# Kernel optimization log

Measured on AMD Instinct MI355X. Metric: run time of the kernel, lower is better.

The kernel has to match this reference:

```python
import jax, jax.numpy as jnp
import numpy as np

V, E, H, K, B, T = 50000, 128, 256, 9, 128, 512
HD = H // 2  # hidden per direction


def setup_inputs() -> dict:
    key = jax.random.key(0)
    ks = jax.random.split(key, 16)
    s = 0.1
    inp = {
        "x": jax.random.randint(ks[0], (B, T), 0, V),
        "emb": jax.random.normal(ks[1], (V, E), jnp.float32) * 0.02,
        "w_ih_f": jax.random.normal(ks[2], (4 * HD, E), jnp.float32) * s,
        "w_hh_f": jax.random.normal(ks[3], (4 * HD, HD), jnp.float32) * s,
        "b_ih_f": jax.random.normal(ks[4], (4 * HD,), jnp.float32) * s,
        "b_hh_f": jax.random.normal(ks[5], (4 * HD,), jnp.float32) * s,
        "w_ih_b": jax.random.normal(ks[6], (4 * HD, E), jnp.float32) * s,
        "w_hh_b": jax.random.normal(ks[7], (4 * HD, HD), jnp.float32) * s,
        "b_ih_b": jax.random.normal(ks[8], (4 * HD,), jnp.float32) * s,
        "b_hh_b": jax.random.normal(ks[9], (4 * HD,), jnp.float32) * s,
        "W_tag": jax.random.normal(ks[10], (K, H), jnp.float32) * s,
        "b_tag": jax.random.normal(ks[11], (K,), jnp.float32) * s,
        "start_trans": jax.random.normal(ks[12], (K,), jnp.float32) * s,
        "end_trans": jax.random.normal(ks[13], (K,), jnp.float32) * s,
        "trans": jax.random.normal(ks[14], (K, K), jnp.float32) * s,
    }
    return inp


def _lstm_dir(xs, w_ih, w_hh, b_ih, b_hh, reverse):
    # xs: [T, B, E]; PyTorch gate order: i, f, g, o
    Bsz = xs.shape[1]
    hd = w_hh.shape[1]
    b = b_ih + b_hh

    def step(carry, x_t):
        h, c = carry
        gates = x_t @ w_ih.T + h @ w_hh.T + b  # [B, 4*hd]
        i, f, g, o = jnp.split(gates, 4, axis=-1)
        i = jax.nn.sigmoid(i)
        f = jax.nn.sigmoid(f)
        g = jnp.tanh(g)
        o = jax.nn.sigmoid(o)
        c = f * c + i * g
        h = o * jnp.tanh(c)
        return (h, c), h

    init = (jnp.zeros((Bsz, hd), xs.dtype), jnp.zeros((Bsz, hd), xs.dtype))
    _, hs = jax.lax.scan(step, init, xs, reverse=reverse)
    return hs  # [T, B, hd], time-ordered


def _viterbi(emissions, start_trans, end_trans, trans):
    # emissions: [T, B, K]; returns best tag path [B, T] (torchcrf decode, no mask)
    score0 = start_trans[None, :] + emissions[0]  # [B, K]

    def step(score, emis_t):
        # score[b, i] + trans[i, j] -> best over i
        cand = score[:, :, None] + trans[None, :, :]  # [B, K, K]
        bp = jnp.argmax(cand, axis=1)                 # [B, K] best prev tag
        best = jnp.max(cand, axis=1)
        return best + emis_t, bp

    final_score, bps = jax.lax.scan(step, score0, emissions[1:])  # bps: [T-1, B, K]
    final_score = final_score + end_trans[None, :]
    last_tag = jnp.argmax(final_score, axis=-1)  # [B]

    def back(tag, bp):
        prev = jnp.take_along_axis(bp, tag[:, None], axis=1)[:, 0]
        return prev, prev

    _, path = jax.lax.scan(back, last_tag, bps, reverse=True)  # [T-1, B]
    tags = jnp.concatenate([path, last_tag[None, :]], axis=0)  # [T, B]
    return tags.T.astype(jnp.int32)  # [B, T]


def reference(x, emb, w_ih_f, w_hh_f, b_ih_f, b_hh_f,
              w_ih_b, w_hh_b, b_ih_b, b_hh_b,
              W_tag, b_tag, start_trans, end_trans, trans):
    xt = x.T                        # [T, B]
    e = emb[xt]                     # [T, B, E] embedding gather
    h_f = _lstm_dir(e, w_ih_f, w_hh_f, b_ih_f, b_hh_f, reverse=False)
    h_b = _lstm_dir(e, w_ih_b, w_hh_b, b_ih_b, b_hh_b, reverse=True)
    h = jnp.concatenate([h_f, h_b], axis=-1)  # [T, B, H]
    # dropout is identity at inference
    emissions = h @ W_tag.T + b_tag           # [T, B, K]
    return _viterbi(emissions, start_trans, end_trans, trans)
```

## Files before the change

kernel.cpp:

```cpp
#include <hip/hip_runtime.h>
#include <math.h>

#define TT 512
#define BB 128
#define KK 9

__device__ __forceinline__ float fast_sigmoid(float x) {
    const float LOG2E = 1.4426950408889634f;
    float e = __builtin_amdgcn_exp2f(-x * LOG2E);
    return __builtin_amdgcn_rcpf(1.0f + e);
}
__device__ __forceinline__ float fast_tanh(float x) {
    const float LOG2E = 1.4426950408889634f;
    float a = fabsf(x);
    float e = __builtin_amdgcn_exp2f(-2.0f * a * LOG2E);
    float t = (1.0f - e) * __builtin_amdgcn_rcpf(1.0f + e);
    return copysignf(t, x);
}

__global__ __launch_bounds__(256, 3) void input_gemm(
    const int* __restrict__ x, const float* __restrict__ emb,
    const float* __restrict__ w_ih_f, const float* __restrict__ w_ih_b,
    const float* __restrict__ b_ih_f, const float* __restrict__ b_hh_f,
    const float* __restrict__ b_ih_b, const float* __restrict__ b_hh_b,
    float* __restrict__ buf_f, float* __restrict__ buf_b,
    int t0f, int t0b)
{
    const int dir = blockIdx.z;
    const int s   = blockIdx.x;
    const int n0  = blockIdx.y * 128;
    const int t   = (dir ? t0b : t0f) + s;
    const float* w  = dir ? w_ih_b : w_ih_f;
    const float* bi = dir ? b_ih_b : b_ih_f;
    const float* bh = dir ? b_hh_b : b_hh_f;
    float* dst = dir ? buf_b : buf_f;

    __shared__ __align__(16) float As[32][132];
    __shared__ __align__(16) float Bs[32][132];

    const int tid  = threadIdx.x;
    const int lrow = tid >> 3;
    const int k4   = (tid & 7) * 4;

    int tokr[4];
    #pragma unroll
    for (int p = 0; p < 4; p++) tokr[p] = x[(p * 32 + lrow) * TT + t];

    const int tx = tid & 15;
    const int ty = tid >> 4;

    float acc[8][8];
    #pragma unroll
    for (int i = 0; i < 8; i++)
        #pragma unroll
        for (int j = 0; j < 8; j++) acc[i][j] = 0.0f;

    float4 aS[4], bS[4];
    #pragma unroll
    for (int p = 0; p < 4; p++) {
        aS[p] = *(const float4*)(emb + (size_t)tokr[p] * 128 + k4);
        bS[p] = *(const float4*)(w + (size_t)(n0 + p * 32 + lrow) * 128 + k4);
    }

    for (int kc = 0; kc < 128; kc += 32) {
        __syncthreads();
        #pragma unroll
        for (int p = 0; p < 4; p++) {
            const int row = p * 32 + lrow;
            As[k4 + 0][row] = aS[p].x; As[k4 + 1][row] = aS[p].y;
            As[k4 + 2][row] = aS[p].z; As[k4 + 3][row] = aS[p].w;
            Bs[k4 + 0][row] = bS[p].x; Bs[k4 + 1][row] = bS[p].y;
            Bs[k4 + 2][row] = bS[p].z; Bs[k4 + 3][row] = bS[p].w;
        }
        __syncthreads();
        if (kc + 32 < 128) {
            #pragma unroll
            for (int p = 0; p < 4; p++) {
                aS[p] = *(const float4*)(emb + (size_t)tokr[p] * 128 + kc + 32 + k4);
                bS[p] = *(const float4*)(w + (size_t)(n0 + p * 32 + lrow) * 128 + kc + 32 + k4);
            }
        }
        #pragma unroll 8
        for (int k = 0; k < 32; k++) {
            float4 af0 = *(const float4*)&As[k][ty * 8];
            float4 af1 = *(const float4*)&As[k][ty * 8 + 4];
            float4 bf0 = *(const float4*)&Bs[k][tx * 8];
            float4 bf1 = *(const float4*)&Bs[k][tx * 8 + 4];
            float a_[8] = {af0.x, af0.y, af0.z, af0.w, af1.x, af1.y, af1.z, af1.w};
            float b_[8] = {bf0.x, bf0.y, bf0.z, bf0.w, bf1.x, bf1.y, bf1.z, bf1.w};
            #pragma unroll
            for (int i = 0; i < 8; i++)
                #pragma unroll
                for (int j = 0; j < 8; j++)
                    acc[i][j] += a_[i] * b_[j];
        }
    }

    const int nbase = n0 + tx * 8;
    float bias[8];
    #pragma unroll
    for (int j = 0; j < 8; j++) {
        int n = nbase + j;
        bias[j] = bi[n] + bh[n];
    }
    #pragma unroll
    for (int i = 0; i < 8; i++) {
        int brow = ty * 8 + i;
        float* o = dst + ((size_t)s * 128 + brow) * 512 + nbase;
        float4 v0, v1;
        v0.x = acc[i][0] + bias[0]; v0.y = acc[i][1] + bias[1];
        v0.z = acc[i][2] + bias[2]; v0.w = acc[i][3] + bias[3];
        v1.x = acc[i][4] + bias[4]; v1.y = acc[i][5] + bias[5];
        v1.z = acc[i][6] + bias[6]; v1.w = acc[i][7] + bias[7];
        *(float4*)o = v0;
        *(float4*)(o + 4) = v1;
    }
}

__global__ __launch_bounds__(512, 2) void lstm_fused(
    const float* __restrict__ buf_f, const float* __restrict__ buf_b,
    const float* __restrict__ w_hh_f, const float* __restrict__ w_hh_b,
    float* __restrict__ h_all,
    float* __restrict__ h_state, float* __restrict__ c_state,
    const float* __restrict__ W_tag, const float* __restrict__ b_tag,
    const float* __restrict__ start_trans, const float* __restrict__ end_trans,
    const float* __restrict__ trans,
    float* __restrict__ emB, unsigned* __restrict__ flags,
    int* __restrict__ out,
    int t0f, int t0b, int C, int init, int tail)
{
    const int dir = blockIdx.x >> 7;
    const int b   = blockIdx.x & 127;
    const int j   = threadIdx.x;
    const int w_  = j >> 6;
    const int l   = j & 63;
    const int m   = l >> 2;
    const int q   = l & 3;
    const int k   = w_ * 16 + m;
    const int r   = q * 128 + k;

    unsigned snap = 0u;
    if (tail && dir == 0 && j == 0)
        snap = __hip_atomic_load(&flags[b], __ATOMIC_RELAXED, __HIP_MEMORY_SCOPE_AGENT);

    const float* whh = dir ? w_hh_b : w_hh_f;
    float wR[128];
    #pragma unroll
    for (int qq = 0; qq < 32; qq++) {
        float4 v = *(const float4*)(whh + (size_t)r * 128 + qq * 4);
        wR[4*qq+0] = v.x; wR[4*qq+1] = v.y; wR[4*qq+2] = v.z; wR[4*qq+3] = v.w;
    }

    __shared__ __align__(16) float h_lds[2][128];
    float c;
    if (init) {
        c = 0.0f;
        if (q == 0) h_lds[0][k] = 0.0f;
    } else {
        c = c_state[((size_t)dir * 128 + b) * 128 + k];
        if (q == 0) h_lds[0][k] = h_state[((size_t)dir * 128 + b) * 128 + k];
    }
    __syncthreads();

    const float* buf = dir ? buf_b : buf_f;
    const int t0     = dir ? t0b : t0f;
    const int  tl0   = dir ? (C - 1) : 0;
    const long lstep = dir ? -(long)(128 * 512) : (long)(128 * 512);

    const float* xp = buf + ((size_t)tl0 * 128 + b) * 512 + r;
    float xw = *xp;
    float h_reg = 0.0f;

    for (int s = 0; s < C; s++) {
        const int t = t0 + (dir ? (C - 1 - s) : s);
        const int p = s & 1;
        const float* hprev = h_lds[p];

        float a0 = 0.f, a1 = 0.f, a2 = 0.f, a3 = 0.f;
        #pragma unroll
        for (int qq = 0; qq < 32; qq++) {
            float4 h4 = *(const float4*)&hprev[4 * qq];
            a0 += wR[4*qq+0] * h4.x;
            a1 += wR[4*qq+1] * h4.y;
            a2 += wR[4*qq+2] * h4.z;
            a3 += wR[4*qq+3] * h4.w;
        }
        float pre = xw + ((a0 + a1) + (a2 + a3));

        float act = (q == 2) ? fast_tanh(pre) : fast_sigmoid(pre);

        float f_ = __shfl_xor(act, 1);
        float g_ = __shfl_xor(act, 2);
        float o_ = __shfl_xor(act, 3);

        c = f_ * c + act * g_;
        h_reg = o_ * fast_tanh(c);
        if (q == 0) h_lds[p ^ 1][k] = h_reg;

        __syncthreads();

        if (s + 1 < C) { xp += lstep; xw = *xp; }
        if (q == 0)
            h_all[((size_t)t * BB + b) * 256 + dir * 128 + k] = h_reg;
    }

    if (q == 0) {
        h_state[((size_t)dir * 128 + b) * 128 + k] = h_reg;
        c_state[((size_t)dir * 128 + b) * 128 + k] = c;
    }

    if (!tail) return;

    __shared__ __align__(16) float wt_s[KK * 128];
    __shared__ __align__(16) float em_s[TT * KK];
    __shared__ unsigned char bp[TT][KK];

    for (int f = j; f < KK * 128; f += 512)
        wt_s[f] = W_tag[(f >> 7) * 256 + dir * 128 + (f & 127)];
    __syncthreads();

    {
        const int t = j;
        const float* hrow = h_all + ((size_t)t * BB + b) * 256 + dir * 128;
        float acc[KK];
        #pragma unroll
        for (int kk = 0; kk < KK; kk++) acc[kk] = 0.0f;
        #pragma unroll 4
        for (int j4 = 0; j4 < 128; j4 += 4) {
            float4 h4 = *(const float4*)(hrow + j4);
            #pragma unroll
            for (int kk = 0; kk < KK; kk++) {
                float4 wv = *(const float4*)&wt_s[kk * 128 + j4];
                acc[kk] += h4.x * wv.x + h4.y * wv.y + h4.z * wv.z + h4.w * wv.w;
            }
        }
        if (dir == 1) {
            float* e = emB + ((size_t)b * TT + t) * KK;
            #pragma unroll
            for (int kk = 0; kk < KK; kk++) e[kk] = acc[kk];
        } else {
            #pragma unroll
            for (int kk = 0; kk < KK; kk++)
                em_s[t * KK + kk] = acc[kk] + b_tag[kk];
        }
    }

    if (dir == 1) {
        __syncthreads();
        if (j == 0) {
            __threadfence();
            __hip_atomic_fetch_add(&flags[b], 1u, __ATOMIC_RELEASE,
                                   __HIP_MEMORY_SCOPE_AGENT);
        }
        return;
    }

    if (j == 0) {
        while (__hip_atomic_load(&flags[b], __ATOMIC_ACQUIRE,
                                 __HIP_MEMORY_SCOPE_AGENT) == snap)
            __builtin_amdgcn_s_sleep(1);
    }
    __syncthreads();
    for (int f = j; f < TT * KK; f += 512)
        em_s[f] += emB[(size_t)b * TT * KK + f];
    __syncthreads();

    if (j < 64) {
        const int lane = j;

        float trans_col[KK];
        float score = -1e30f;
        if (lane < KK) {
            #pragma unroll
            for (int i = 0; i < KK; i++) trans_col[i] = trans[i * KK + lane];
            score = start_trans[lane] + em_s[lane];
        }

        float em_cur = (lane < KK) ? em_s[KK + lane] : 0.0f;
        for (int t = 1; t < TT; t++) {
            float em_next = (t + 1 < TT && lane < KK) ? em_s[(t + 1) * KK + lane] : 0.0f;

            float my = (lane < KK) ? score : -1e30f;
            float cand[KK];
            #pragma unroll
            for (int i = 0; i < KK; i++) cand[i] = __shfl(my, i) + trans_col[i];

            float v01, v23, v45, v67, v03, v47, v07, vb_;
            int   i01, i23, i45, i67, i03, i47, i07, ib_;
            {
                bool gt;
                gt = cand[1] > cand[0]; v01 = gt ? cand[1] : cand[0]; i01 = gt ? 1 : 0;
                gt = cand[3] > cand[2]; v23 = gt ? cand[3] : cand[2]; i23 = gt ? 3 : 2;
                gt = cand[5] > cand[4]; v45 = gt ? cand[5] : cand[4]; i45 = gt ? 5 : 4;
                gt = cand[7] > cand[6]; v67 = gt ? cand[7] : cand[6]; i67 = gt ? 7 : 6;
                gt = v23 > v01; v03 = gt ? v23 : v01; i03 = gt ? i23 : i01;
                gt = v67 > v45; v47 = gt ? v67 : v45; i47 = gt ? i67 : i45;
                gt = v47 > v03; v07 = gt ? v47 : v03; i07 = gt ? i47 : i03;
                gt = cand[8] > v07; vb_ = gt ? cand[8] : v07; ib_ = gt ? 8 : i07;
            }

            if (lane < KK) {
                bp[t][lane] = (unsigned char)ib_;
                score = vb_ + em_cur;
            }
            em_cur = em_next;
        }

        float fin = (lane < KK) ? (score + end_trans[lane]) : -1e30f;
        float farr[KK];
        #pragma unroll
        for (int jx = 0; jx < KK; jx++) farr[jx] = __shfl(fin, jx);
        float v01, v23, v45, v67, v03, v47, v07, vb_;
        int   i01, i23, i45, i67, i03, i47, i07, bj;
        {
            bool gt;
            gt = farr[1] > farr[0]; v01 = gt ? farr[1] : farr[0]; i01 = gt ? 1 : 0;
            gt = farr[3] > farr[2]; v23 = gt ? farr[3] : farr[2]; i23 = gt ? 3 : 2;
            gt = farr[5] > farr[4]; v45 = gt ? farr[5] : farr[4]; i45 = gt ? 5 : 4;
            gt = farr[7] > farr[6]; v67 = gt ? farr[7] : farr[6]; i67 = gt ? 7 : 6;
            gt = v23 > v01; v03 = gt ? v23 : v01; i03 = gt ? i23 : i01;
            gt = v67 > v45; v47 = gt ? v67 : v45; i47 = gt ? i67 : i45;
            gt = v47 > v03; v07 = gt ? v47 : v03; i07 = gt ? i47 : i03;
            gt = farr[8] > v07; vb_ = gt ? farr[8] : v07; bj = gt ? 8 : i07;
        }

        if (lane == 0) {
            int tag = bj;
            out[b * TT + (TT - 1)] = tag;
            for (int t = TT - 1; t >= 1; t--) {
                tag = bp[t][tag];
                out[b * TT + t - 1] = tag;
            }
        }
    }
}

extern "C" void kernel_launch(void* const* d_in, const int* in_sizes, int n_in,
                              void* d_out, int out_size, void* d_ws, size_t ws_size,
                              hipStream_t stream)
{
    const int*   x       = (const int*)  d_in[0];
    const float* emb     = (const float*)d_in[1];
    const float* w_ih_f  = (const float*)d_in[2];
    const float* w_hh_f  = (const float*)d_in[3];
    const float* b_ih_f  = (const float*)d_in[4];
    const float* b_hh_f  = (const float*)d_in[5];
    const float* w_ih_b  = (const float*)d_in[6];
    const float* w_hh_b  = (const float*)d_in[7];
    const float* b_ih_b  = (const float*)d_in[8];
    const float* b_hh_b  = (const float*)d_in[9];
    const float* W_tag   = (const float*)d_in[10];
    const float* b_tag   = (const float*)d_in[11];
    const float* start_t = (const float*)d_in[12];
    const float* end_t   = (const float*)d_in[13];
    const float* trans   = (const float*)d_in[14];
    int* out = (int*)d_out;

    const size_t hall_elems  = (size_t)TT * BB * 256;
    const size_t emB_elems   = (size_t)BB * TT * KK;
    const size_t state_elems = (size_t)2 * 128 * 128;

    int C = 32;
    const int cands[5] = {512, 256, 128, 64, 32};
    for (int ci = 0; ci < 5; ci++) {
        size_t need = ((size_t)2 * cands[ci] * BB * 512
                       + hall_elems + emB_elems
                       + 2 * state_elems) * sizeof(float) + 512;
        if (ws_size >= need) { C = cands[ci]; break; }
    }

    float* buf_f   = (float*)d_ws;
    float* buf_b   = buf_f + (size_t)C * BB * 512;
    float* emB     = buf_b + (size_t)C * BB * 512;
    float* h_state = emB + emB_elems;
    float* c_state = h_state + state_elems;
    float* h_all   = c_state + state_elems;
    unsigned* flags = (unsigned*)(h_all + hall_elems);

    const int rounds = TT / C;
    for (int r = 0; r < rounds; r++) {
        const int t0f = r * C;
        const int t0b = TT - (r + 1) * C;
        dim3 gg(C, 4, 2);
        input_gemm<<<gg, dim3(256), 0, stream>>>(
            x, emb, w_ih_f, w_ih_b, b_ih_f, b_hh_f, b_ih_b, b_hh_b,
            buf_f, buf_b, t0f, t0b);
        lstm_fused<<<dim3(256), dim3(512), 0, stream>>>(
            buf_f, buf_b, w_hh_f, w_hh_b, h_all,
            h_state, c_state,
            W_tag, b_tag, start_t, end_t, trans,
            emB, flags, out,
            t0f, t0b, C, (r == 0) ? 1 : 0, (r == rounds - 1) ? 1 : 0);
    }
}
```

Before: 887.8 us.

## Compute tag emissions inside LSTM recurrence instead of storing full hidden states

After: 1.694 ms. 90.9% more time.

```diff
diff --git a/kernel.cpp b/kernel.cpp
--- a/kernel.cpp
+++ b/kernel.cpp
@@ -120,13 +120,12 @@
 __global__ __launch_bounds__(512, 2) void lstm_fused(
     const float* __restrict__ buf_f, const float* __restrict__ buf_b,
     const float* __restrict__ w_hh_f, const float* __restrict__ w_hh_b,
-    float* __restrict__ h_all,
     float* __restrict__ h_state, float* __restrict__ c_state,
     const float* __restrict__ W_tag, const float* __restrict__ b_tag,
     const float* __restrict__ start_trans, const float* __restrict__ end_trans,
     const float* __restrict__ trans,
-    float* __restrict__ emB, unsigned* __restrict__ flags,
-    int* __restrict__ out,
+    float* __restrict__ emF, float* __restrict__ emB,
+    unsigned* __restrict__ flags, int* __restrict__ out,
     int t0f, int t0b, int C, int init, int tail)
 {
     const int dir = blockIdx.x >> 7;
@@ -152,6 +151,13 @@
     }
 
     __shared__ __align__(16) float h_lds[2][128];
+    __shared__ __align__(16) float wt_s[KK * 128];
+    __shared__ __align__(16) float em_s[TT * KK];
+    __shared__ unsigned char bp[TT][KK];
+
+    for (int f = j; f < KK * 128; f += 512)
+        wt_s[f] = W_tag[(f >> 7) * 256 + dir * 128 + (f & 127)];
+
     float c;
     if (init) {
         c = 0.0f;
@@ -171,8 +177,12 @@
     float xw = *xp;
     float h_reg = 0.0f;
 
+    const int  eg  = j >> 4;
+    const int  el  = j & 15;
+    const bool edo = (eg < KK);
+    float* emdst = (dir ? emB : emF) + (size_t)b * TT * KK;
+
     for (int s = 0; s < C; s++) {
-        const int t = t0 + (dir ? (C - 1 - s) : s);
         const int p = s & 1;
         const float* hprev = h_lds[p];
 
@@ -187,6 +197,21 @@
         }
         float pre = xw + ((a0 + a1) + (a2 + a3));
 
+        if (edo && s) {
+            const int tprev = t0 + (dir ? (C - s) : (s - 1));
+            const float4 hA = *(const float4*)&hprev[el * 8];
+            const float4 hB = *(const float4*)&hprev[el * 8 + 4];
+            const float4 wA = *(const float4*)&wt_s[eg * 128 + el * 8];
+            const float4 wB = *(const float4*)&wt_s[eg * 128 + el * 8 + 4];
+            float pp = hA.x*wA.x + hA.y*wA.y + hA.z*wA.z + hA.w*wA.w
+                     + hB.x*wB.x + hB.y*wB.y + hB.z*wB.z + hB.w*wB.w;
+            pp += __shfl_xor(pp, 8);
+            pp += __shfl_xor(pp, 4);
+            pp += __shfl_xor(pp, 2);
+            pp += __shfl_xor(pp, 1);
+            if (el == 0) emdst[(size_t)tprev * KK + eg] = pp;
+        }
+
         float act = (q == 2) ? fast_tanh(pre) : fast_sigmoid(pre);
 
         float f_ = __shfl_xor(act, 1);
@@ -200,8 +225,22 @@
         __syncthreads();
 
         if (s + 1 < C) { xp += lstep; xw = *xp; }
-        if (q == 0)
-            h_all[((size_t)t * BB + b) * 256 + dir * 128 + k] = h_reg;
+    }
+
+    if (edo) {
+        const int tlast = t0 + (dir ? 0 : (C - 1));
+        const float* hp = h_lds[C & 1];
+        const float4 hA = *(const float4*)&hp[el * 8];
+        const float4 hB = *(const float4*)&hp[el * 8 + 4];
+        const float4 wA = *(const float4*)&wt_s[eg * 128 + el * 8];
+        const float4 wB = *(const float4*)&wt_s[eg * 128 + el * 8 + 4];
+        float pp = hA.x*wA.x + hA.y*wA.y + hA.z*wA.z + hA.w*wA.w
+                 + hB.x*wB.x + hB.y*wB.y + hB.z*wB.z + hB.w*wB.w;
+        pp += __shfl_xor(pp, 8);
+        pp += __shfl_xor(pp, 4);
+        pp += __shfl_xor(pp, 2);
+        pp += __shfl_xor(pp, 1);
+        if (el == 0) emdst[(size_t)tlast * KK + eg] = pp;
     }
 
     if (q == 0) {
@@ -210,40 +249,6 @@
     }
 
     if (!tail) return;
-
-    __shared__ __align__(16) float wt_s[KK * 128];
-    __shared__ __align__(16) float em_s[TT * KK];
-    __shared__ unsigned char bp[TT][KK];
-
-    for (int f = j; f < KK * 128; f += 512)
-        wt_s[f] = W_tag[(f >> 7) * 256 + dir * 128 + (f & 127)];
-    __syncthreads();
-
-    {
-        const int t = j;
-        const float* hrow = h_all + ((size_t)t * BB + b) * 256 + dir * 128;
-        float acc[KK];
-        #pragma unroll
-        for (int kk = 0; kk < KK; kk++) acc[kk] = 0.0f;
-        #pragma unroll 4
-        for (int j4 = 0; j4 < 128; j4 += 4) {
-            float4 h4 = *(const float4*)(hrow + j4);
-            #pragma unroll
-            for (int kk = 0; kk < KK; kk++) {
-                float4 wv = *(const float4*)&wt_s[kk * 128 + j4];
-                acc[kk] += h4.x * wv.x + h4.y * wv.y + h4.z * wv.z + h4.w * wv.w;
-            }
-        }
-        if (dir == 1) {
-            float* e = emB + ((size_t)b * TT + t) * KK;
-            #pragma unroll
-            for (int kk = 0; kk < KK; kk++) e[kk] = acc[kk];
-        } else {
-            #pragma unroll
-            for (int kk = 0; kk < KK; kk++)
-                em_s[t * KK + kk] = acc[kk] + b_tag[kk];
-        }
-    }
 
     if (dir == 1) {
         __syncthreads();
@@ -261,8 +266,12 @@
             __builtin_amdgcn_s_sleep(1);
     }
     __syncthreads();
-    for (int f = j; f < TT * KK; f += 512)
-        em_s[f] += emB[(size_t)b * TT * KK + f];
+    {
+        const float* eF = emF + (size_t)b * TT * KK;
+        const float* eB = emB + (size_t)b * TT * KK;
+        for (int f = j; f < TT * KK; f += 512)
+            em_s[f] = eF[f] + eB[f] + b_tag[f % KK];
+    }
     __syncthreads();
 
     if (j < 64) {
@@ -356,26 +365,24 @@
     const float* trans   = (const float*)d_in[14];
     int* out = (int*)d_out;
 
-    const size_t hall_elems  = (size_t)TT * BB * 256;
-    const size_t emB_elems   = (size_t)BB * TT * KK;
+    const size_t em_elems    = (size_t)BB * TT * KK;
     const size_t state_elems = (size_t)2 * 128 * 128;
 
     int C = 32;
     const int cands[5] = {512, 256, 128, 64, 32};
     for (int ci = 0; ci < 5; ci++) {
         size_t need = ((size_t)2 * cands[ci] * BB * 512
-                       + hall_elems + emB_elems
-                       + 2 * state_elems) * sizeof(float) + 512;
+                       + 2 * em_elems + 2 * state_elems) * sizeof(float) + 1024;
         if (ws_size >= need) { C = cands[ci]; break; }
     }
 
     float* buf_f   = (float*)d_ws;
     float* buf_b   = buf_f + (size_t)C * BB * 512;
-    float* emB     = buf_b + (size_t)C * BB * 512;
-    float* h_state = emB + emB_elems;
+    float* emF     = buf_b + (size_t)C * BB * 512;
+    float* emB     = emF + em_elems;
+    float* h_state = emB + em_elems;
     float* c_state = h_state + state_elems;
-    float* h_all   = c_state + state_elems;
-    unsigned* flags = (unsigned*)(h_all + hall_elems);
+    unsigned* flags = (unsigned*)(c_state + state_elems);
 
     const int rounds = TT / C;
     for (int r = 0; r < rounds; r++) {
@@ -386,10 +393,10 @@
             x, emb, w_ih_f, w_ih_b, b_ih_f, b_hh_f, b_ih_b, b_hh_b,
             buf_f, buf_b, t0f, t0b);
         lstm_fused<<<dim3(256), dim3(512), 0, stream>>>(
-            buf_f, buf_b, w_hh_f, w_hh_b, h_all,
+            buf_f, buf_b, w_hh_f, w_hh_b,
             h_state, c_state,
             W_tag, b_tag, start_t, end_t, trans,
-            emB, flags, out,
+            emF, emB, flags, out,
             t0f, t0b, C, (r == 0) ? 1 : 0, (r == rounds - 1) ? 1 : 0);
     }
 }
```

## Store LSTM hidden states per batch-direction and tile emission projection through LDS

Applied to the files above, without the earlier changes.

Result: faster. 855.8 us (-3.6%).

```diff
diff --git a/kernel.cpp b/kernel.cpp
--- a/kernel.cpp
+++ b/kernel.cpp
@@ -152,6 +152,11 @@
     }
 
     __shared__ __align__(16) float h_lds[2][128];
+    __shared__ __align__(16) float wt_s[KK * 132];
+    __shared__ __align__(16) float em_s[TT * KK];
+    __shared__ __align__(16) float h_tile[64 * 132];
+    __shared__ unsigned char bp[TT][KK];
+
     float c;
     if (init) {
         c = 0.0f;
@@ -170,6 +175,8 @@
     const float* xp = buf + ((size_t)tl0 * 128 + b) * 512 + r;
     float xw = *xp;
     float h_reg = 0.0f;
+
+    float* hdst = h_all + (size_t)(dir * BB + b) * TT * 128;
 
     for (int s = 0; s < C; s++) {
         const int t = t0 + (dir ? (C - 1 - s) : s);
@@ -201,7 +208,7 @@
 
         if (s + 1 < C) { xp += lstep; xw = *xp; }
         if (q == 0)
-            h_all[((size_t)t * BB + b) * 256 + dir * 128 + k] = h_reg;
+            hdst[(size_t)t * 128 + k] = h_reg;
     }
 
     if (q == 0) {
@@ -211,42 +218,42 @@
 
     if (!tail) return;
 
-    __shared__ __align__(16) float wt_s[KK * 128];
-    __shared__ __align__(16) float em_s[TT * KK];
-    __shared__ unsigned char bp[TT][KK];
-
     for (int f = j; f < KK * 128; f += 512)
-        wt_s[f] = W_tag[(f >> 7) * 256 + dir * 128 + (f & 127)];
+        wt_s[(f >> 7) * 132 + (f & 127)] = W_tag[(f >> 7) * 256 + dir * 128 + (f & 127)];
+
+    float* emdst = emB + (size_t)b * TT * KK;
+
+    for (int tile = 0; tile < TT / 64; tile++) {
+        const int tb = tile * 64;
+        __syncthreads();
+        #pragma unroll
+        for (int it = 0; it < 4; it++) {
+            const int f4 = it * 512 + j;
+            const int tr = f4 >> 5;
+            const int c4 = (f4 & 31) * 4;
+            float4 v = *(const float4*)(hdst + (size_t)(tb + tr) * 128 + c4);
+            *(float4*)&h_tile[tr * 132 + c4] = v;
+        }
+        __syncthreads();
+        for (int task = j; task < 64 * KK; task += 512) {
+            const int tl = task / 9;
+            const int kk = task - tl * 9;
+            const float* hp = &h_tile[tl * 132];
+            const float* wp = &wt_s[kk * 132];
+            float acc = 0.0f;
+            #pragma unroll
+            for (int i4 = 0; i4 < 32; i4++) {
+                float4 h4 = *(const float4*)(hp + i4 * 4);
+                float4 w4 = *(const float4*)(wp + i4 * 4);
+                acc += h4.x * w4.x + h4.y * w4.y + h4.z * w4.z + h4.w * w4.w;
+            }
+            if (dir == 1) emdst[(size_t)tb * KK + task] = acc;
+            else          em_s[tb * KK + task] = acc;
+        }
+    }
     __syncthreads();
 
-    {
-        const int t = j;
-        const float* hrow = h_all + ((size_t)t * BB + b) * 256 + dir * 128;
-        float acc[KK];
-        #pragma unroll
-        for (int kk = 0; kk < KK; kk++) acc[kk] = 0.0f;
-        #pragma unroll 4
-        for (int j4 = 0; j4 < 128; j4 += 4) {
-            float4 h4 = *(const float4*)(hrow + j4);
-            #pragma unroll
-            for (int kk = 0; kk < KK; kk++) {
-                float4 wv = *(const float4*)&wt_s[kk * 128 + j4];
-                acc[kk] += h4.x * wv.x + h4.y * wv.y + h4.z * wv.z + h4.w * wv.w;
-            }
-        }
-        if (dir == 1) {
-            float* e = emB + ((size_t)b * TT + t) * KK;
-            #pragma unroll
-            for (int kk = 0; kk < KK; kk++) e[kk] = acc[kk];
-        } else {
-            #pragma unroll
-            for (int kk = 0; kk < KK; kk++)
-                em_s[t * KK + kk] = acc[kk] + b_tag[kk];
-        }
-    }
-
     if (dir == 1) {
-        __syncthreads();
         if (j == 0) {
             __threadfence();
             __hip_atomic_fetch_add(&flags[b], 1u, __ATOMIC_RELEASE,
@@ -262,7 +269,7 @@
     }
     __syncthreads();
     for (int f = j; f < TT * KK; f += 512)
-        em_s[f] += emB[(size_t)b * TT * KK + f];
+        em_s[f] += emdst[f] + b_tag[f % KK];
     __syncthreads();
 
     if (j < 64) {
@@ -356,23 +363,23 @@
     const float* trans   = (const float*)d_in[14];
     int* out = (int*)d_out;
 
-    const size_t hall_elems  = (size_t)TT * BB * 256;
-    const size_t emB_elems   = (size_t)BB * TT * KK;
+    const size_t em_elems    = (size_t)BB * TT * KK;
     const size_t state_elems = (size_t)2 * 128 * 128;
+    const size_t hall_elems  = (size_t)2 * BB * TT * 128;
 
     int C = 32;
     const int cands[5] = {512, 256, 128, 64, 32};
     for (int ci = 0; ci < 5; ci++) {
         size_t need = ((size_t)2 * cands[ci] * BB * 512
-                       + hall_elems + emB_elems
-                       + 2 * state_elems) * sizeof(float) + 512;
+                       + em_elems + 2 * state_elems + hall_elems) * sizeof(float)
+                      + 1024;
         if (ws_size >= need) { C = cands[ci]; break; }
     }
 
     float* buf_f   = (float*)d_ws;
     float* buf_b   = buf_f + (size_t)C * BB * 512;
     float* emB     = buf_b + (size_t)C * BB * 512;
-    float* h_state = emB + emB_elems;
+    float* h_state = emB + em_elems;
     float* c_state = h_state + state_elems;
     float* h_all   = c_state + state_elems;
     unsigned* flags = (unsigned*)(h_all + hall_elems);
```
